# Performance work log

Measured on AMD Instinct MI355X. Metric: run time of the kernel, lower is better.

The kernel has to match this reference:

```python
import jax, jax.numpy as jnp
import numpy as np
from jax import lax

# ---- constants matching init_kwargs ----
NY, NX = 1024, 1024
DX, DY = 50.0, 50.0
TTOT = 32.0
DTMAX = 0.5
RHO, G, FD = 910.0, 9.81, 1e-17
EPS = 1e-10
T_FREQ = 5.0
N_STEPS = 64            # fixed step count (>= TTOT/DTMAX); dt masked to 0 once time >= TTOT
LAPSE = 0.0065          # degC per m elevation lapse rate (SMB model)
MELT_FACTOR = 0.5       # m ice / (degC * yr) ablation factor (SMB model)


def update_smb(Z_surf, precip, T_ma_lowest, T_mj_lowest, ice_mask):
    # Lapse-rate temperatures at the surface
    T_ma = T_ma_lowest - LAPSE * Z_surf   # mean annual temperature
    T_mj = T_mj_lowest - LAPSE * Z_surf   # mean July temperature
    accumulation = precip * (T_ma < 0.0).astype(Z_surf.dtype)
    ablation = MELT_FACTOR * jnp.maximum(T_mj, 0.0)
    return (accumulation - ablation) * ice_mask


def setup_inputs() -> dict:
    key = jax.random.key(0)
    k1, k2, k3 = jax.random.split(key, 3)
    # smooth mountain topography: 2500 m gaussian massif + small noise
    y = np.arange(NY, dtype=np.float32) * DY
    x = np.arange(NX, dtype=np.float32) * DX
    yy, xx = np.meshgrid(y, x, indexing="ij")
    cy, cx = y.mean(), x.mean()
    sigma = 0.25 * NX * DX
    z = 2500.0 * np.exp(-((yy - cy) ** 2 + (xx - cx) ** 2) / (2.0 * sigma ** 2))
    Z_topo = jnp.asarray(z, dtype=jnp.float32) + 5.0 * jax.random.normal(k1, (NY, NX), dtype=jnp.float32)
    precip_tensor = 2.0 * jax.random.uniform(k2, (NY, NX), dtype=jnp.float32)  # m ice / yr
    T_ma_lowest = jnp.float32(8.0) + jax.random.normal(k3, (), dtype=jnp.float32)
    T_mj_lowest = T_ma_lowest + jnp.float32(8.0)
    ice_mask = jnp.ones((NY, NX), dtype=jnp.float32)
    return {"precip_tensor": precip_tensor, "T_ma_lowest": T_ma_lowest,
            "T_mj_lowest": T_mj_lowest, "Z_topo": Z_topo, "ice_mask": ice_mask}


def _glacier_step(carry, _, Z_topo, precip, T_ma_lowest, T_mj_lowest, ice_mask):
    H_ice, Z_surf, smb, time, t_last = carry
    # staggered-grid averages and slopes (SIA diffusion)
    H_avg = 0.25 * (H_ice[:-1, :-1] + H_ice[1:, 1:] + H_ice[:-1, 1:] + H_ice[1:, :-1])
    Sx = (Z_surf[:, 1:] - Z_surf[:, :-1]) / DX
    Sy = (Z_surf[1:, :] - Z_surf[:-1, :]) / DY
    Sx = 0.5 * (Sx[:-1, :] + Sx[1:, :])          # (NY-1, NX-1)
    Sy = 0.5 * (Sy[:, :-1] + Sy[:, 1:])          # (NY-1, NX-1)
    Snorm = jnp.sqrt(Sx ** 2 + Sy ** 2 + EPS)
    D = FD * (RHO * G) ** 3 * H_avg ** 5 * Snorm ** 2 + EPS
    # adaptive CFL dt; torch uses .item() so dt is a non-differentiable constant
    dt = jnp.minimum(min(DX, DY) ** 2 / (2.7 * jnp.max(D)), DTMAX)
    dt = lax.stop_gradient(dt)
    dt = jnp.where(time < TTOT, dt, 0.0)         # freeze once ttot is reached
    qx = -(0.5 * (D[:-1, :] + D[1:, :])) * (Z_surf[1:-1, 1:] - Z_surf[1:-1, :-1]) / DX
    qy = -(0.5 * (D[:, :-1] + D[:, 1:])) * (Z_surf[1:, 1:-1] - Z_surf[:-1, 1:-1]) / DY
    dHdt = -(jnp.diff(qx, axis=1) / DX + jnp.diff(qy, axis=0) / DY)  # (NY-2, NX-2)
    H_new = H_ice.at[1:-1, 1:-1].add(dt * (dHdt + smb[1:-1, 1:-1]))
    H_new = jnp.maximum(H_new, 0.0)
    Z_new = Z_topo + H_new
    time = time + dt
    # refresh SMB every T_FREQ model years
    do_upd = (time - t_last) >= T_FREQ
    smb_new = update_smb(Z_new, precip, T_ma_lowest, T_mj_lowest, ice_mask)
    smb = jnp.where(do_upd, smb_new, smb)
    t_last = jnp.where(do_upd, time, t_last)
    return (H_new, Z_new, smb, time, t_last), None


def reference(precip_tensor, T_ma_lowest, T_mj_lowest, Z_topo, ice_mask):
    H_ice = jnp.zeros((NY, NX), dtype=jnp.float32)
    Z_surf = Z_topo + H_ice
    smb = update_smb(Z_surf, precip_tensor, T_ma_lowest, T_mj_lowest, ice_mask)
    time = jnp.float32(0.0)
    t_last = jnp.float32(0.0)
    step = lambda c, x: _glacier_step(c, x, Z_topo, precip_tensor, T_ma_lowest, T_mj_lowest, ice_mask)
    (H_ice, _, _, _, _), _ = lax.scan(step, (H_ice, Z_surf, smb, time, t_last), None, length=N_STEPS)
    return H_ice
```

## Files before the change

### kernel.cpp

```cpp
#include <hip/hip_runtime.h>
#include <math.h>

#define NYg 1024
#define NXg 1024
#define W   1024
#define NSTEPS 64
#define GRID_N (NYg * W)

#define SLOT_STRIDE 32
#define SLOT_GROUP  256
#define NSLOTG      (NSTEPS + 1)
#define WS_CNT  (NSLOTG * SLOT_GROUP)
#define WS_NBF  (WS_CNT + 8 * 32)
#define WS_CTRL_END (WS_NBF + 256 * 32)
#define WS_GRIDS 32768

constexpr float DXf   = 50.0f;
constexpr float DYf   = 50.0f;
constexpr float TTOTf = 32.0f;
constexpr float DTMAXf= 0.5f;
constexpr float EPSf  = 1e-10f;
constexpr float TFREQ = 5.0f;
constexpr float LAPSE = 0.0065f;
constexpr float MELTF = 0.5f;
constexpr double RHOG = 910.0 * 9.81;
constexpr float  CDf  = (float)(1e-17 * RHOG * RHOG * RHOG);

__device__ __forceinline__ float scloadf(const float* p) {
    return __hip_atomic_load(p, __ATOMIC_RELAXED, __HIP_MEMORY_SCOPE_SYSTEM);
}
__device__ __forceinline__ void scstoref(float* p, float v) {
    __hip_atomic_store(p, v, __ATOMIC_RELAXED, __HIP_MEMORY_SCOPE_SYSTEM);
}
__device__ __forceinline__ unsigned scloadu(const unsigned* p) {
    return __hip_atomic_load(p, __ATOMIC_RELAXED, __HIP_MEMORY_SCOPE_SYSTEM);
}

__device__ __forceinline__ float dfunc(float h00, float h01, float h10, float h11,
                                       float z00, float z01, float z10, float z11)
{
    float havg = 0.25f * (h00 + h11 + h01 + h10);
    float sx = ((z01 - z00) + (z11 - z10)) * (0.5f / DXf);
    float sy = ((z10 - z00) + (z11 - z01)) * (0.5f / DYf);
    float sn = sqrtf(sx * sx + sy * sy + EPSf);
    float h2 = havg * havg;
    float h4 = h2 * h2;
    return CDf * (h4 * havg) * (sn * sn) + EPSf;
}

__global__ __launch_bounds__(256) void k_init(unsigned* __restrict__ ctrl)
{
    int idx = blockIdx.x * blockDim.x + threadIdx.x;
    int stride = gridDim.x * blockDim.x;
    for (int i = idx; i < WS_CTRL_END; i += stride) {
        unsigned v = 0u;
        if (i < SLOT_GROUP && (i & (SLOT_STRIDE - 1)) == 0) v = __float_as_uint(EPSf);
        ctrl[i] = v;
    }
}

__global__ __launch_bounds__(1024, 1) void k_run(
    float* __restrict__ EZ0, float* __restrict__ EZ1,
    float* __restrict__ ED0, float* __restrict__ ED1,
    const float* __restrict__ ztopo, const float* __restrict__ precip,
    const float* __restrict__ mask, const float* __restrict__ tma,
    const float* __restrict__ tmj, unsigned* __restrict__ ctrl,
    float* __restrict__ Hout)
{
    __shared__ float sZ[7][W];
    __shared__ float sHm[5][W];
    __shared__ float sD[6][W];
    __shared__ unsigned su[8];
    __shared__ float smax16[16];

    unsigned* slots = ctrl;
    unsigned* cnt   = ctrl + WS_CNT;
    unsigned* nbf   = ctrl + WS_NBF;

    const int c   = threadIdx.x;
    const int b   = blockIdx.x;
    const int r0  = b * 4;
    const int grp = b & 7;
    const int lane = c & 63, wid = c >> 6;
    const bool hasA = (b > 0), hasB = (b < 255);

    const float TMA = tma[0], TMJ = tmj[0];

    float smbr[5], ztr[5], hN[5];

    #pragma unroll
    for (int q = 0; q < 7; ++q) {
        int r = r0 - 1 + q;
        sZ[q][c] = (r >= 0 && r < NYg) ? ztopo[r * W + c] : 0.0f;
    }
    #pragma unroll
    for (int q = 0; q < 5; ++q) sHm[q][c] = 0.0f;
    #pragma unroll
    for (int q = 0; q < 6; ++q) sD[q][c] = EPSf;
    #pragma unroll
    for (int rr = 0; rr < 5; ++rr) {
        int r = r0 + rr;
        if (r < NYg) {
            float z = ztopo[r * W + c];
            ztr[rr] = z;
            float t_ma = TMA - LAPSE * z;
            float t_mj = TMJ - LAPSE * z;
            float acc  = (t_ma < 0.0f) ? precip[r * W + c] : 0.0f;
            float abl  = MELTF * fmaxf(t_mj, 0.0f);
            smbr[rr] = (acc - abl) * mask[r * W + c];
        } else { ztr[rr] = 0.0f; smbr[rr] = 0.0f; }
    }
    __syncthreads();

    float t = 0.0f, tl = 0.0f;

    for (int s = 0; s < NSTEPS; ++s) {
        const float* EZr = (s & 1) ? EZ1 : EZ0;
        float*       EZw = (s & 1) ? EZ0 : EZ1;
        const float* EDr = (s & 1) ? ED1 : ED0;
        float*       EDw = (s & 1) ? ED0 : ED1;

        if (s > 0) {
            if (c == 0 && hasA)
                while (scloadu(&nbf[(b - 1) * 32]) < (unsigned)s) __builtin_amdgcn_s_sleep(1);
            if (c == 64 && hasB)
                while (scloadu(&nbf[(b + 1) * 32]) < (unsigned)s) __builtin_amdgcn_s_sleep(1);
            __syncthreads();
            if (hasA) { sZ[0][c] = scloadf(EZr + (r0 - 1) * W + c);
                        if (c <= NXg - 2) sD[0][c] = scloadf(EDr + (r0 - 1) * W + c); }
            if (hasB) { sZ[6][c] = scloadf(EZr + (r0 + 5) * W + c);
                        if (c <= NXg - 2) sD[5][c] = scloadf(EDr + (r0 + 4) * W + c); }
            __syncthreads();
        }

        float dh[5], hOld[5], zOld[5];
        bool inter[5];
        #pragma unroll
        for (int rr = 0; rr < 5; ++rr) {
            int r = r0 + rr;
            float zc = 0.0f, hc = 0.0f, d = 0.0f;
            bool iv = false;
            if (r < NYg) {
                zc = sZ[rr + 1][c];
                hc = sHm[rr][c];
                iv = (r >= 1 && r <= NYg - 2 && c >= 1 && c <= NXg - 2);
                if (iv) {
                    float zl = sZ[rr + 1][c - 1], zr = sZ[rr + 1][c + 1];
                    float zt = sZ[rr][c],         zb = sZ[rr + 2][c];
                    float d00 = sD[rr][c - 1],     d01 = sD[rr][c];
                    float d10 = sD[rr + 1][c - 1], d11 = sD[rr + 1][c];
                    float qxR = -0.5f * (d01 + d11) * (zr - zc) * (1.0f / DXf);
                    float qxL = -0.5f * (d00 + d10) * (zc - zl) * (1.0f / DXf);
                    float qyB = -0.5f * (d10 + d11) * (zb - zc) * (1.0f / DYf);
                    float qyT = -0.5f * (d00 + d01) * (zc - zt) * (1.0f / DYf);
                    d = -((qxR - qxL) * (1.0f / DXf) + (qyB - qyT) * (1.0f / DYf));
                }
            }
            dh[rr] = d; hOld[rr] = hc; zOld[rr] = zc; inter[rr] = iv;
        }

        if (c < 8) {
            unsigned tgt = 32u * (unsigned)s;
            while (scloadu(&cnt[c * 32]) < tgt) __builtin_amdgcn_s_sleep(1);
            su[c] = scloadu(&slots[s * SLOT_GROUP + c * SLOT_STRIDE]);
        }
        __syncthreads();

        unsigned mb = su[0];
        #pragma unroll
        for (int q = 1; q < 8; ++q) mb = max(mb, su[q]);
        float mD = __uint_as_float(mb);
        float dt = fminf(2500.0f / (2.7f * mD), DTMAXf);
        if (!(t < TTOTf)) dt = 0.0f;
        float nt  = t + dt;
        bool  upd = (nt - tl) >= TFREQ;

        #pragma unroll
        for (int rr = 0; rr < 5; ++rr) {
            int r = r0 + rr;
            float h, z;
            if (r >= NYg)        { h = 0.0f; z = 0.0f; }
            else if (inter[rr])  { h = fmaxf(hOld[rr] + dt * (dh[rr] + smbr[rr]), 0.0f);
                                   z = ztr[rr] + h; }
            else                 { h = 0.0f; z = zOld[rr]; }
            hN[rr] = h;
            if (r < NYg) {
                sZ[rr + 1][c] = z;
                sHm[rr][c]    = h;
                if (rr == 1 && hasA) scstoref(EZw + r * W + c, z);
                if (rr == 3 && hasB) scstoref(EZw + r * W + c, z);
                if (upd) {
                    float t_ma = TMA - LAPSE * z;
                    float t_mj = TMJ - LAPSE * z;
                    float acc  = (t_ma < 0.0f) ? precip[r * W + c] : 0.0f;
                    float abl  = MELTF * fmaxf(t_mj, 0.0f);
                    smbr[rr] = (acc - abl) * mask[r * W + c];
                }
            }
        }
        __syncthreads();

        if (s < NSTEPS - 1) {
            float m = 0.0f;
            #pragma unroll
            for (int rr = 0; rr < 4; ++rr) {
                int i = r0 + rr;
                if (i <= NYg - 2 && c <= NXg - 2) {
                    float d = dfunc(sHm[rr][c], sHm[rr][c + 1],
                                    sHm[rr + 1][c], sHm[rr + 1][c + 1],
                                    sZ[rr + 1][c], sZ[rr + 1][c + 1],
                                    sZ[rr + 2][c], sZ[rr + 2][c + 1]);
                    sD[rr + 1][c] = d;
                    m = fmaxf(m, d);
                    if (rr == 0 && hasA) scstoref(EDw + i * W + c, d);
                    if (rr == 3 && hasB) scstoref(EDw + i * W + c, d);
                }
            }
            asm volatile("s_waitcnt vmcnt(0)" ::: "memory");
            #pragma unroll
            for (int off = 32; off >= 1; off >>= 1)
                m = fmaxf(m, __shfl_xor(m, off, 64));
            if (lane == 0) smax16[wid] = m;
            __syncthreads();
            if (c == 0) {
                #pragma unroll
                for (int q = 1; q < 16; ++q) m = fmaxf(m, smax16[q]);
                __hip_atomic_fetch_max(&slots[(s + 1) * SLOT_GROUP + grp * SLOT_STRIDE],
                                       __float_as_uint(m),
                                       __ATOMIC_RELAXED, __HIP_MEMORY_SCOPE_SYSTEM);
                asm volatile("s_waitcnt vmcnt(0)" ::: "memory");
                __hip_atomic_fetch_add(&cnt[grp * 32], 1u,
                                       __ATOMIC_RELAXED, __HIP_MEMORY_SCOPE_SYSTEM);
                __hip_atomic_store(&nbf[b * 32], (unsigned)(s + 1),
                                   __ATOMIC_RELAXED, __HIP_MEMORY_SCOPE_SYSTEM);
            }
        }

        t = nt;
        if (upd) tl = nt;
    }

    #pragma unroll
    for (int rr = 0; rr < 4; ++rr)
        Hout[(r0 + rr) * W + c] = hN[rr];
}

extern "C" void kernel_launch(void* const* d_in, const int* in_sizes, int n_in,
                              void* d_out, int out_size, void* d_ws, size_t ws_size,
                              hipStream_t stream)
{
    const float* precip = (const float*)d_in[0];
    const float* tma    = (const float*)d_in[1];
    const float* tmj    = (const float*)d_in[2];
    const float* ztopo  = (const float*)d_in[3];
    const float* mask   = (const float*)d_in[4];

    unsigned* ctrl = (unsigned*)d_ws;
    float* g = (float*)d_ws + WS_GRIDS;
    float* EZ0 = g + 0 * GRID_N;
    float* EZ1 = g + 1 * GRID_N;
    float* ED0 = g + 2 * GRID_N;
    float* ED1 = g + 3 * GRID_N;

    k_init<<<dim3(64), dim3(256), 0, stream>>>(ctrl);

    k_run<<<dim3(256), dim3(1024), 0, stream>>>(EZ0, EZ1, ED0, ED1,
                                                ztopo, precip, mask, tma, tmj,
                                                ctrl, (float*)d_out);
}
```

Before: 461.4 us.

## Keep per-thread stencil column in registers and compact halo exchange buffers

Moves each thread's own column of Z, H and D values into registers, and keeps only the neighbour-column data in packed shared arrays (float2 Z/H, float4 D). This cuts LDS traffic and per-step shared-memory rewrites. The halo exchange now uses compact per-block edge buffers (a/b) instead of full-grid arrays, and the global max of D is reduced with wave shuffles instead of a serial loop. The s_waitcnt is moved later so stores can overlap the shuffle reduction, at the cost of higher register pressure.

```diff
diff --git a/kernel.cpp b/kernel.cpp
--- a/kernel.cpp
+++ b/kernel.cpp
@@ -5,7 +5,8 @@
 #define NXg 1024
 #define W   1024
 #define NSTEPS 64
-#define GRID_N (NYg * W)
+#define NBLK 256
+#define EN (NBLK * W)
 
 #define SLOT_STRIDE 32
 #define SLOT_GROUP  256
@@ -60,18 +61,21 @@
 }
 
 __global__ __launch_bounds__(1024, 1) void k_run(
-    float* __restrict__ EZ0, float* __restrict__ EZ1,
-    float* __restrict__ ED0, float* __restrict__ ED1,
+    float* __restrict__ EZa0, float* __restrict__ EZa1,
+    float* __restrict__ EZb0, float* __restrict__ EZb1,
+    float* __restrict__ EDa0, float* __restrict__ EDa1,
+    float* __restrict__ EDb0, float* __restrict__ EDb1,
     const float* __restrict__ ztopo, const float* __restrict__ precip,
     const float* __restrict__ mask, const float* __restrict__ tma,
     const float* __restrict__ tmj, unsigned* __restrict__ ctrl,
     float* __restrict__ Hout)
 {
-    __shared__ float sZ[7][W];
-    __shared__ float sHm[5][W];
-    __shared__ float sD[6][W];
-    __shared__ unsigned su[8];
-    __shared__ float smax16[16];
+    __shared__ float2 sZH[5][W];
+    __shared__ float4 sDT[W];
+    __shared__ float  sDtop[W];
+    __shared__ float  sDbot[W];
+    __shared__ float  smax16[16];
+    __shared__ float  sMD;
 
     unsigned* slots = ctrl;
     unsigned* cnt   = ctrl + WS_CNT;
@@ -82,43 +86,58 @@
     const int r0  = b * 4;
     const int grp = b & 7;
     const int lane = c & 63, wid = c >> 6;
-    const bool hasA = (b > 0), hasB = (b < 255);
+    const bool hasA = (b > 0), hasB = (b < NBLK - 1);
+    const bool cL = (c >= 1), cR = (c <= NXg - 2);
 
     const float TMA = tma[0], TMJ = tmj[0];
 
-    float smbr[5], ztr[5], hN[5];
+    float z_[7];
+    float h_[5];
+    float dreg[4];
+    float dtop, dbot;
+    float smbr[5], ztr[5];
 
     #pragma unroll
     for (int q = 0; q < 7; ++q) {
         int r = r0 - 1 + q;
-        sZ[q][c] = (r >= 0 && r < NYg) ? ztopo[r * W + c] : 0.0f;
+        z_[q] = (r >= 0 && r < NYg) ? ztopo[r * W + c] : 0.0f;
     }
-    #pragma unroll
-    for (int q = 0; q < 5; ++q) sHm[q][c] = 0.0f;
-    #pragma unroll
-    for (int q = 0; q < 6; ++q) sD[q][c] = EPSf;
     #pragma unroll
     for (int rr = 0; rr < 5; ++rr) {
         int r = r0 + rr;
+        h_[rr] = 0.0f;
         if (r < NYg) {
-            float z = ztopo[r * W + c];
+            float z = z_[rr + 1];
             ztr[rr] = z;
             float t_ma = TMA - LAPSE * z;
             float t_mj = TMJ - LAPSE * z;
             float acc  = (t_ma < 0.0f) ? precip[r * W + c] : 0.0f;
             float abl  = MELTF * fmaxf(t_mj, 0.0f);
             smbr[rr] = (acc - abl) * mask[r * W + c];
-        } else { ztr[rr] = 0.0f; smbr[rr] = 0.0f; }
+            sZH[rr][c] = make_float2(z, 0.0f);
+        } else {
+            ztr[rr] = 0.0f; smbr[rr] = 0.0f;
+            sZH[rr][c] = make_float2(0.0f, 0.0f);
+        }
     }
+    dtop = EPSf; dbot = EPSf;
+    #pragma unroll
+    for (int q = 0; q < 4; ++q) dreg[q] = EPSf;
+    sDT[c] = make_float4(EPSf, EPSf, EPSf, EPSf);
+    sDtop[c] = EPSf; sDbot[c] = EPSf;
     __syncthreads();
 
     float t = 0.0f, tl = 0.0f;
 
     for (int s = 0; s < NSTEPS; ++s) {
-        const float* EZr = (s & 1) ? EZ1 : EZ0;
-        float*       EZw = (s & 1) ? EZ0 : EZ1;
-        const float* EDr = (s & 1) ? ED1 : ED0;
-        float*       EDw = (s & 1) ? ED0 : ED1;
+        const float* EZar = (s & 1) ? EZa1 : EZa0;
+        float*       EZaw = (s & 1) ? EZa0 : EZa1;
+        const float* EZbr = (s & 1) ? EZb1 : EZb0;
+        float*       EZbw = (s & 1) ? EZb0 : EZb1;
+        const float* EDar = (s & 1) ? EDa1 : EDa0;
+        float*       EDaw = (s & 1) ? EDa0 : EDa1;
+        const float* EDbr = (s & 1) ? EDb1 : EDb0;
+        float*       EDbw = (s & 1) ? EDb0 : EDb1;
 
         if (s > 0) {
             if (c == 0 && hasA)
@@ -126,50 +145,58 @@
             if (c == 64 && hasB)
                 while (scloadu(&nbf[(b + 1) * 32]) < (unsigned)s) __builtin_amdgcn_s_sleep(1);
             __syncthreads();
-            if (hasA) { sZ[0][c] = scloadf(EZr + (r0 - 1) * W + c);
-                        if (c <= NXg - 2) sD[0][c] = scloadf(EDr + (r0 - 1) * W + c); }
-            if (hasB) { sZ[6][c] = scloadf(EZr + (r0 + 5) * W + c);
-                        if (c <= NXg - 2) sD[5][c] = scloadf(EDr + (r0 + 4) * W + c); }
+            if (hasA) {
+                z_[0] = scloadf(EZbr + (b - 1) * W + c);
+                if (cR) { float v = scloadf(EDbr + (b - 1) * W + c); dtop = v; sDtop[c] = v; }
+            }
+            if (hasB) {
+                z_[6] = scloadf(EZar + (b + 1) * W + c);
+                if (cR) { float v = scloadf(EDar + (b + 1) * W + c); dbot = v; sDbot[c] = v; }
+            }
             __syncthreads();
         }
 
-        float dh[5], hOld[5], zOld[5];
-        bool inter[5];
+        float dh[5];
+        bool  inter[5];
+        float4 dTl = make_float4(0.0f, 0.0f, 0.0f, 0.0f);
+        float dtl = 0.0f, dbl = 0.0f;
+        if (cL) { dTl = sDT[c - 1]; dtl = sDtop[c - 1]; dbl = sDbot[c - 1]; }
+        float dla[6], doa[6];
+        dla[0] = dtl;  dla[1] = dTl.x; dla[2] = dTl.y; dla[3] = dTl.z; dla[4] = dTl.w; dla[5] = dbl;
+        doa[0] = dtop; doa[1] = dreg[0]; doa[2] = dreg[1]; doa[3] = dreg[2]; doa[4] = dreg[3]; doa[5] = dbot;
         #pragma unroll
         for (int rr = 0; rr < 5; ++rr) {
             int r = r0 + rr;
-            float zc = 0.0f, hc = 0.0f, d = 0.0f;
-            bool iv = false;
-            if (r < NYg) {
-                zc = sZ[rr + 1][c];
-                hc = sHm[rr][c];
-                iv = (r >= 1 && r <= NYg - 2 && c >= 1 && c <= NXg - 2);
-                if (iv) {
-                    float zl = sZ[rr + 1][c - 1], zr = sZ[rr + 1][c + 1];
-                    float zt = sZ[rr][c],         zb = sZ[rr + 2][c];
-                    float d00 = sD[rr][c - 1],     d01 = sD[rr][c];
-                    float d10 = sD[rr + 1][c - 1], d11 = sD[rr + 1][c];
-                    float qxR = -0.5f * (d01 + d11) * (zr - zc) * (1.0f / DXf);
-                    float qxL = -0.5f * (d00 + d10) * (zc - zl) * (1.0f / DXf);
-                    float qyB = -0.5f * (d10 + d11) * (zb - zc) * (1.0f / DYf);
-                    float qyT = -0.5f * (d00 + d01) * (zc - zt) * (1.0f / DYf);
-                    d = -((qxR - qxL) * (1.0f / DXf) + (qyB - qyT) * (1.0f / DYf));
-                }
-            }
-            dh[rr] = d; hOld[rr] = hc; zOld[rr] = zc; inter[rr] = iv;
+            float d = 0.0f;
+            bool iv = (r >= 1 && r <= NYg - 2 && cL && cR);
+            if (iv) {
+                float zc  = z_[rr + 1];
+                float zl  = sZH[rr][c - 1].x;
+                float zr2 = sZH[rr][c + 1].x;
+                float zt  = z_[rr], zb = z_[rr + 2];
+                float d00 = dla[rr],     d01 = doa[rr];
+                float d10 = dla[rr + 1], d11 = doa[rr + 1];
+                float qxR = -0.5f * (d01 + d11) * (zr2 - zc) * (1.0f / DXf);
+                float qxL = -0.5f * (d00 + d10) * (zc - zl) * (1.0f / DXf);
+                float qyB = -0.5f * (d10 + d11) * (zb - zc) * (1.0f / DYf);
+                float qyT = -0.5f * (d00 + d01) * (zc - zt) * (1.0f / DYf);
+                d = -((qxR - qxL) * (1.0f / DXf) + (qyB - qyT) * (1.0f / DYf));
+            }
+            dh[rr] = d; inter[rr] = iv;
         }
 
         if (c < 8) {
             unsigned tgt = 32u * (unsigned)s;
             while (scloadu(&cnt[c * 32]) < tgt) __builtin_amdgcn_s_sleep(1);
-            su[c] = scloadu(&slots[s * SLOT_GROUP + c * SLOT_STRIDE]);
+            float v = __uint_as_float(scloadu(&slots[s * SLOT_GROUP + c * SLOT_STRIDE]));
+            v = fmaxf(v, __shfl_xor(v, 4, 64));
+            v = fmaxf(v, __shfl_xor(v, 2, 64));
+            v = fmaxf(v, __shfl_xor(v, 1, 64));
+            if (c == 0) sMD = v;
         }
         __syncthreads();
 
-        unsigned mb = su[0];
-        #pragma unroll
-        for (int q = 1; q < 8; ++q) mb = max(mb, su[q]);
-        float mD = __uint_as_float(mb);
+        float mD = sMD;
         float dt = fminf(2500.0f / (2.7f * mD), DTMAXf);
         if (!(t < TTOTf)) dt = 0.0f;
         float nt  = t + dt;
@@ -178,17 +205,15 @@
         #pragma unroll
         for (int rr = 0; rr < 5; ++rr) {
             int r = r0 + rr;
-            float h, z;
-            if (r >= NYg)        { h = 0.0f; z = 0.0f; }
-            else if (inter[rr])  { h = fmaxf(hOld[rr] + dt * (dh[rr] + smbr[rr]), 0.0f);
-                                   z = ztr[rr] + h; }
-            else                 { h = 0.0f; z = zOld[rr]; }
-            hN[rr] = h;
             if (r < NYg) {
-                sZ[rr + 1][c] = z;
-                sHm[rr][c]    = h;
-                if (rr == 1 && hasA) scstoref(EZw + r * W + c, z);
-                if (rr == 3 && hasB) scstoref(EZw + r * W + c, z);
+                float h, z;
+                if (inter[rr]) { h = fmaxf(h_[rr] + dt * (dh[rr] + smbr[rr]), 0.0f);
+                                 z = ztr[rr] + h; }
+                else           { h = 0.0f; z = z_[rr + 1]; }
+                h_[rr] = h; z_[rr + 1] = z;
+                sZH[rr][c] = make_float2(z, h);
+                if (rr == 1 && hasA) scstoref(EZaw + b * W + c, z);
+                if (rr == 3 && hasB) scstoref(EZbw + b * W + c, z);
                 if (upd) {
                     float t_ma = TMA - LAPSE * z;
                     float t_mj = TMJ - LAPSE * z;
@@ -196,31 +221,43 @@
                     float abl  = MELTF * fmaxf(t_mj, 0.0f);
                     smbr[rr] = (acc - abl) * mask[r * W + c];
                 }
+            } else {
+                h_[rr] = 0.0f;
             }
         }
         __syncthreads();
 
         if (s < NSTEPS - 1) {
+            float2 zh1[5];
+            if (cR) {
+                #pragma unroll
+                for (int q = 0; q < 5; ++q) zh1[q] = sZH[q][c + 1];
+            } else {
+                #pragma unroll
+                for (int q = 0; q < 5; ++q) zh1[q] = make_float2(0.0f, 0.0f);
+            }
             float m = 0.0f;
+            float dv[4];
             #pragma unroll
             for (int rr = 0; rr < 4; ++rr) {
                 int i = r0 + rr;
-                if (i <= NYg - 2 && c <= NXg - 2) {
-                    float d = dfunc(sHm[rr][c], sHm[rr][c + 1],
-                                    sHm[rr + 1][c], sHm[rr + 1][c + 1],
-                                    sZ[rr + 1][c], sZ[rr + 1][c + 1],
-                                    sZ[rr + 2][c], sZ[rr + 2][c + 1]);
-                    sD[rr + 1][c] = d;
-                    m = fmaxf(m, d);
-                    if (rr == 0 && hasA) scstoref(EDw + i * W + c, d);
-                    if (rr == 3 && hasB) scstoref(EDw + i * W + c, d);
+                float dd = 0.0f;
+                if (i <= NYg - 2 && cR) {
+                    dd = dfunc(h_[rr], zh1[rr].y, h_[rr + 1], zh1[rr + 1].y,
+                               z_[rr + 1], zh1[rr].x, z_[rr + 2], zh1[rr + 1].x);
+                    m = fmaxf(m, dd);
+                    if (rr == 0 && hasA) scstoref(EDaw + b * W + c, dd);
+                    if (rr == 3 && hasB) scstoref(EDbw + b * W + c, dd);
                 }
-            }
-            asm volatile("s_waitcnt vmcnt(0)" ::: "memory");
+                dv[rr] = dd;
+            }
+            sDT[c] = make_float4(dv[0], dv[1], dv[2], dv[3]);
+            dreg[0] = dv[0]; dreg[1] = dv[1]; dreg[2] = dv[2]; dreg[3] = dv[3];
             #pragma unroll
             for (int off = 32; off >= 1; off >>= 1)
                 m = fmaxf(m, __shfl_xor(m, off, 64));
             if (lane == 0) smax16[wid] = m;
+            asm volatile("s_waitcnt vmcnt(0)" ::: "memory");
             __syncthreads();
             if (c == 0) {
                 #pragma unroll
@@ -242,7 +279,7 @@
 
     #pragma unroll
     for (int rr = 0; rr < 4; ++rr)
-        Hout[(r0 + rr) * W + c] = hN[rr];
+        Hout[(r0 + rr) * W + c] = h_[rr];
 }
 
 extern "C" void kernel_launch(void* const* d_in, const int* in_sizes, int n_in,
@@ -257,14 +294,15 @@
 
     unsigned* ctrl = (unsigned*)d_ws;
     float* g = (float*)d_ws + WS_GRIDS;
-    float* EZ0 = g + 0 * GRID_N;
-    float* EZ1 = g + 1 * GRID_N;
-    float* ED0 = g + 2 * GRID_N;
-    float* ED1 = g + 3 * GRID_N;
+    float* EZa0 = g + 0 * EN; float* EZa1 = g + 1 * EN;
+    float* EZb0 = g + 2 * EN; float* EZb1 = g + 3 * EN;
+    float* EDa0 = g + 4 * EN; float* EDa1 = g + 5 * EN;
+    float* EDb0 = g + 6 * EN; float* EDb1 = g + 7 * EN;
 
     k_init<<<dim3(64), dim3(256), 0, stream>>>(ctrl);
 
-    k_run<<<dim3(256), dim3(1024), 0, stream>>>(EZ0, EZ1, ED0, ED1,
+    k_run<<<dim3(256), dim3(1024), 0, stream>>>(EZa0, EZa1, EZb0, EZb1,
+                                                EDa0, EDa1, EDb0, EDb1,
                                                 ztopo, precip, mask, tma, tmj,
                                                 ctrl, (float*)d_out);
 }
```

New measurement: 490.7 us. 6.3% more time.
